# Kernel optimization log

Hardware: AMD Instinct MI355X
Metric: run time of the kernel (lower is better)

## Reference

```python
import jax, jax.numpy as jnp
import numpy as np

B, T, C, H, KV, D = 2, 2048, 1024, 16, 4, 64
VE_GATE_CH = 32


def _rope(x, cos, sin):
    # x: (B,T,h,D); cos/sin: (1,T,1,D//2); half-split rotary
    d = x.shape[-1] // 2
    x1, x2 = x[..., :d], x[..., d:]
    return jnp.concatenate([x1 * cos + x2 * sin, -x1 * sin + x2 * cos], axis=-1)


def _rms_norm(x, eps=1.1920929e-07):
    # F.rms_norm with no weight; eps defaults to finfo(fp32).eps
    return x * jax.lax.rsqrt(jnp.mean(x * x, axis=-1, keepdims=True) + eps)


def setup_inputs() -> dict:
    key = jax.random.key(0)
    ks = jax.random.split(key, 8)
    x = jax.random.normal(ks[0], (B, T, C), dtype=jnp.float32)
    ve = jax.random.normal(ks[1], (B, T, KV * D), dtype=jnp.float32)
    # standard RoPE tables, half-dim = D//2
    inv_freq = 1.0 / (10000.0 ** (np.arange(0, D, 2, dtype=np.float32) / D))  # (32,)
    freqs = np.arange(T, dtype=np.float32)[:, None] * inv_freq[None, :]       # (T,32)
    cos = jnp.asarray(np.cos(freqs))[None, :, None, :]
    sin = jnp.asarray(np.sin(freqs))[None, :, None, :]
    s = 0.02
    Wq = jax.random.normal(ks[2], (C, H * D), dtype=jnp.float32) * s
    Wk = jax.random.normal(ks[3], (C, KV * D), dtype=jnp.float32) * s
    Wv = jax.random.normal(ks[4], (C, KV * D), dtype=jnp.float32) * s
    Wo = jax.random.normal(ks[5], (C, C), dtype=jnp.float32) * s
    Wg = jax.random.normal(ks[6], (VE_GATE_CH, KV), dtype=jnp.float32) * s
    return {"x": x, "ve": ve, "cos": cos, "sin": sin,
            "Wq": Wq, "Wk": Wk, "Wv": Wv, "Wo": Wo, "Wg": Wg,
            "window": 1024}


def reference(x, ve, cos, sin, Wq, Wk, Wv, Wo, Wg, window):
    b, t, c = x.shape
    q = (x @ Wq).reshape(b, t, H, D)
    k = (x @ Wk).reshape(b, t, KV, D)
    v = (x @ Wv).reshape(b, t, KV, D)
    # value-embedding gating: gate = 2*sigmoid(x[..., :32] @ Wg)
    gate = 2.0 * jax.nn.sigmoid(x[..., :VE_GATE_CH] @ Wg)  # (B,T,KV)
    v = v + gate[..., None] * ve.reshape(b, t, KV, D)
    q = _rms_norm(_rope(q, cos, sin))
    k = _rms_norm(_rope(k, cos, sin))
    # GQA: repeat_interleave kv heads to match query heads
    groups = H // KV
    k = jnp.repeat(k, groups, axis=2)  # (B,T,H,D)
    v = jnp.repeat(v, groups, axis=2)
    scale = 1.0 / jnp.sqrt(jnp.asarray(D, dtype=q.dtype))
    scores = jnp.einsum("bthd,bshd->bhts", q, k) * scale  # (B,H,T,T)
    rows = jnp.arange(t)[:, None]
    cols = jnp.arange(t)[None, :]
    mask = (cols <= rows) & (cols > rows - window)  # causal sliding window
    scores = jnp.where(mask[None, None], scores, jnp.finfo(scores.dtype).min)
    attn = jax.nn.softmax(scores, axis=-1)
    y = jnp.einsum("bhts,bshd->bthd", attn, v).reshape(b, t, c)
    return y @ Wo
```

## Files before the change

kernel.cpp:

```cpp
#include <hip/hip_runtime.h>
#include <hip/hip_bf16.h>

#define B_ 2
#define T_ 2048
#define C_ 1024
#define H_ 16
#define KV_ 4
#define D_ 64
#define M_ (B_*T_)

typedef __attribute__((ext_vector_type(4))) float f32x4;
typedef __attribute__((ext_vector_type(8))) short bf16x8;

__device__ __forceinline__ float exp2fast(float x) {
  return __builtin_amdgcn_exp2f(x);
}

__device__ __forceinline__ unsigned short f2bfu(float f) {
  unsigned u = __builtin_bit_cast(unsigned, f);
  u += 0x7FFFu + ((u >> 16) & 1u);
  return (unsigned short)(u >> 16);
}

__device__ __forceinline__ short f2bf(float f) {
  return (short)f2bfu(f);
}

__device__ __forceinline__ float bf2f(short s) {
  unsigned u = ((unsigned)(unsigned short)s) << 16;
  return __builtin_bit_cast(float, u);
}

__device__ __forceinline__ unsigned cvtpk(float a, float b) {
  unsigned r;
  asm("v_cvt_pk_bf16_f32 %0, %1, %2" : "=v"(r) : "v"(a), "v"(b));
  return r;
}

__device__ __forceinline__ void gld_lds16(const void* g, void* l) {
  __builtin_amdgcn_global_load_lds(
      (const __attribute__((address_space(1))) void*)g,
      (__attribute__((address_space(3))) void*)l, 16, 0, 0);
}

__global__ __launch_bounds__(256) void k_cast(const float* __restrict__ in,
                                              short* __restrict__ out, int n) {
  int i = (blockIdx.x * 256 + threadIdx.x) * 4;
  if (i + 3 < n) {
    float4 f = *(const float4*)(in + i);
    short4 s;
    s.x = f2bf(f.x); s.y = f2bf(f.y); s.z = f2bf(f.z); s.w = f2bf(f.w);
    *(short4*)(out + i) = s;
  }
}

__global__ __launch_bounds__(256) void k_transpose_all(const float* __restrict__ Wq,
                                                       const float* __restrict__ Wk,
                                                       const float* __restrict__ Wv,
                                                       const float* __restrict__ Wo,
                                                       short* __restrict__ wT,
                                                       short* __restrict__ woT) {
  __shared__ float tile[32][33];
  int bx = blockIdx.x;
  const float* in; short* out; int Ncol, cb;
  if (bx < 32)      { in = Wq; out = wT;                       Ncol = 1024; cb = bx; }
  else if (bx < 40) { in = Wk; out = wT + (size_t)1024 * 1024; Ncol = 256;  cb = bx - 32; }
  else if (bx < 48) { in = Wv; out = wT + (size_t)1280 * 1024; Ncol = 256;  cb = bx - 40; }
  else              { in = Wo; out = woT;                      Ncol = 1024; cb = bx - 48; }
  const int R = 1024;
  int c0 = cb * 32, r0 = blockIdx.y * 32;
  int tx = threadIdx.x, ty = threadIdx.y;
#pragma unroll
  for (int i = 0; i < 32; i += 8)
    tile[ty + i][tx] = in[(size_t)(r0 + ty + i) * Ncol + c0 + tx];
  __syncthreads();
#pragma unroll
  for (int i = 0; i < 32; i += 8)
    out[(size_t)(c0 + ty + i) * R + r0 + tx] = f2bf(tile[tx][ty + i]);
}

__global__ __launch_bounds__(256) void k_gemm64(const short* __restrict__ A,
                                                const short* __restrict__ Bt,
                                                float* __restrict__ C,
                                                int M, int N, int K) {
  __shared__ short sA[64 * 64];
  __shared__ short sB[128 * 64];
  const int tid = threadIdx.x;
  const int wid = tid >> 6, lane = tid & 63;
  const int g = lane >> 4, c = lane & 15;
  const int wm = wid >> 1, wn = wid & 1;
  const int m0 = blockIdx.y * 64, n0 = blockIdx.x * 128;
  const int strow = tid >> 3;
  const int scol  = ((tid & 7) ^ (strow & 7)) * 8;
  const int sw = c & 7;

  const short* Ag = A + (size_t)(m0 + strow) * K + scol;
  const short* Bg = Bt + (size_t)(n0 + strow) * K + scol;
  const int ldbase = wid * 512;

  f32x4 acc[2][4] = {};

  for (int k0 = 0; k0 < K; k0 += 64) {
#pragma unroll
    for (int i = 0; i < 2; ++i)
      gld_lds16(Ag + (size_t)(i * 32) * K + k0, &sA[i * 2048 + ldbase]);
#pragma unroll
    for (int i = 0; i < 4; ++i)
      gld_lds16(Bg + (size_t)(i * 32) * K + k0, &sB[i * 2048 + ldbase]);
    __syncthreads();
#pragma unroll
    for (int kk = 0; kk < 2; ++kk) {
      bf16x8 af[2], bfr[4];
#pragma unroll
      for (int i = 0; i < 2; ++i)
        af[i] = *(const bf16x8*)&sA[(wm * 32 + i * 16 + c) * 64 + ((kk * 4 + g) ^ sw) * 8];
#pragma unroll
      for (int j = 0; j < 4; ++j)
        bfr[j] = *(const bf16x8*)&sB[(wn * 64 + j * 16 + c) * 64 + ((kk * 4 + g) ^ sw) * 8];
#pragma unroll
      for (int i = 0; i < 2; ++i)
#pragma unroll
        for (int j = 0; j < 4; ++j)
          acc[i][j] = __builtin_amdgcn_mfma_f32_16x16x32_bf16(af[i], bfr[j], acc[i][j], 0, 0, 0);
    }
    __syncthreads();
  }
#pragma unroll
  for (int i = 0; i < 2; ++i)
#pragma unroll
    for (int j = 0; j < 4; ++j) {
      int row = m0 + wm * 32 + i * 16 + g * 4;
      int col = n0 + wn * 64 + j * 16 + c;
      float* cp = C + (size_t)row * N + col;
#pragma unroll
      for (int r = 0; r < 4; ++r) cp[(size_t)r * N] = acc[i][j][r];
    }
}

__global__ __launch_bounds__(256) void k_gemm64b(const short* __restrict__ A,
                                                 const short* __restrict__ Bt,
                                                 short* __restrict__ C,
                                                 int M, int N, int K) {
  __shared__ short sA[64 * 64];
  __shared__ short sB[128 * 64];
  const int tid = threadIdx.x;
  const int wid = tid >> 6, lane = tid & 63;
  const int g = lane >> 4, c = lane & 15;
  const int wm = wid >> 1, wn = wid & 1;
  const int m0 = blockIdx.y * 64, n0 = blockIdx.x * 128;
  const int strow = tid >> 3;
  const int scol  = ((tid & 7) ^ (strow & 7)) * 8;
  const int sw = c & 7;

  const short* Ag = A + (size_t)(m0 + strow) * K + scol;
  const short* Bg = Bt + (size_t)(n0 + strow) * K + scol;
  const int ldbase = wid * 512;

  f32x4 acc[2][4] = {};

  for (int k0 = 0; k0 < K; k0 += 64) {
#pragma unroll
    for (int i = 0; i < 2; ++i)
      gld_lds16(Ag + (size_t)(i * 32) * K + k0, &sA[i * 2048 + ldbase]);
#pragma unroll
    for (int i = 0; i < 4; ++i)
      gld_lds16(Bg + (size_t)(i * 32) * K + k0, &sB[i * 2048 + ldbase]);
    __syncthreads();
#pragma unroll
    for (int kk = 0; kk < 2; ++kk) {
      bf16x8 af[2], bfr[4];
#pragma unroll
      for (int i = 0; i < 2; ++i)
        af[i] = *(const bf16x8*)&sA[(wm * 32 + i * 16 + c) * 64 + ((kk * 4 + g) ^ sw) * 8];
#pragma unroll
      for (int j = 0; j < 4; ++j)
        bfr[j] = *(const bf16x8*)&sB[(wn * 64 + j * 16 + c) * 64 + ((kk * 4 + g) ^ sw) * 8];
#pragma unroll
      for (int i = 0; i < 2; ++i)
#pragma unroll
        for (int j = 0; j < 4; ++j)
          acc[i][j] = __builtin_amdgcn_mfma_f32_16x16x32_bf16(af[i], bfr[j], acc[i][j], 0, 0, 0);
    }
    __syncthreads();
  }
#pragma unroll
  for (int i = 0; i < 2; ++i)
#pragma unroll
    for (int j = 0; j < 4; ++j) {
      int row = m0 + wm * 32 + i * 16 + g * 4;
      int col = n0 + wn * 64 + j * 16 + c;
      short* cp = C + (size_t)row * N + col;
#pragma unroll
      for (int r = 0; r < 4; ++r) cp[(size_t)r * N] = f2bf(acc[i][j][r]);
    }
}

__global__ __launch_bounds__(256) void k_post(const short* __restrict__ qkvb,
                                              const float* __restrict__ x,
                                              const float* __restrict__ cosp,
                                              const float* __restrict__ sinp,
                                              const float* __restrict__ Wg,
                                              short* __restrict__ qb,
                                              short* __restrict__ kb,
                                              float* __restrict__ gateb) {
  const int row = blockIdx.x;
  const int b = row >> 11, t = row & (T_ - 1);
  const int wid = threadIdx.x >> 6, lane = threadIdx.x & 63;
  const short* qrow = qkvb + (size_t)row * 1536;
  const float cv = cosp[t * 32 + (lane & 31)];
  const float sv = sinp[t * 32 + (lane & 31)];

  for (int vi = wid; vi < 24; vi += 4) {
    if (vi < 20) {
      float val = bf2f(qrow[vi < 16 ? vi * 64 + lane : 1024 + (vi - 16) * 64 + lane]);
      float other = __shfl_xor(val, 32);
      float r = (lane < 32) ? fmaf(val, cv, other * sv) : fmaf(val, cv, -other * sv);
      float ss = r * r;
      ss += __shfl_xor(ss, 1);  ss += __shfl_xor(ss, 2);  ss += __shfl_xor(ss, 4);
      ss += __shfl_xor(ss, 8);  ss += __shfl_xor(ss, 16); ss += __shfl_xor(ss, 32);
      float outv = r * rsqrtf(ss * (1.0f / 64.0f) + 1.1920929e-07f);
      if (vi < 16)
        qb[((size_t)(b * H_ + vi) * T_ + t) * D_ + lane] = f2bf(outv);
      else
        kb[((size_t)(b * KV_ + (vi - 16)) * T_ + t) * D_ + lane] = f2bf(outv);
    } else {
      int kvh = vi - 20;
      float xg = (lane < 32) ? x[(size_t)row * C_ + lane] * Wg[lane * KV_ + kvh] : 0.0f;
      xg += __shfl_xor(xg, 1);  xg += __shfl_xor(xg, 2);  xg += __shfl_xor(xg, 4);
      xg += __shfl_xor(xg, 8);  xg += __shfl_xor(xg, 16); xg += __shfl_xor(xg, 32);
      if (lane == 0)
        gateb[(size_t)row * KV_ + kvh] = 2.0f / (1.0f + __expf(-xg));
    }
  }
}

__global__ __launch_bounds__(256) void k_vtrans(const short* __restrict__ qkvb,
                                                const float* __restrict__ ve,
                                                const float* __restrict__ gateb,
                                                short* __restrict__ vT) {
  const int t0 = blockIdx.x * 64;
  const int bk = blockIdx.y;
  const int b = bk >> 2, kv = bk & 3;
  const int tx = threadIdx.x;
  const int ty = threadIdx.y;
  __shared__ float tile[64][65];
#pragma unroll
  for (int i = 0; i < 16; ++i) {
    const int tr = ty + 4 * i;
    const int row = b * T_ + t0 + tr;
    float g = gateb[(size_t)row * KV_ + kv];
    float v = bf2f(qkvb[(size_t)row * 1536 + 1280 + kv * 64 + tx]);
    v = fmaf(g, ve[(size_t)row * (KV_ * D_) + kv * 64 + tx], v);
    tile[tr][tx] = v;
  }
  __syncthreads();
#pragma unroll
  for (int i = 0; i < 16; ++i) {
    const int d = ty + 4 * i;
    vT[((size_t)bk * 64 + d) * T_ + t0 + tx] = f2bf(tile[tx][d]);
  }
}

__global__ __launch_bounds__(512, 6) void k_attn(const short* __restrict__ qg,
                                                 const short* __restrict__ kg,
                                                 const short* __restrict__ vg,
                                                 short* __restrict__ yb,
                                                 const int* __restrict__ winp) {
  const int wsz = *winp;
  const int qt = blockIdx.x, bh = blockIdx.y;
  const int b = bh >> 4, h = bh & 15;
  const int kvh = h >> 2;
  const int tid = threadIdx.x;
  const int wid = tid >> 6, lane = tid & 63;
  const int g = lane >> 4, c = lane & 15;
  const int t0 = qt * 128 + wid * 16;

  __shared__ short sK[2][64 * 64];
  __shared__ short sV[2][64 * 64];
  __shared__ short spt_all[8][16][72];
  short (*spt)[72] = spt_all[wid];

  const short* qbase = qg + ((size_t)(b * H_ + h) * T_ + t0) * D_;
  const bf16x8 bq0 = *(const bf16x8*)(qbase + c * D_ + g * 8);
  const bf16x8 bq1 = *(const bf16x8*)(qbase + c * D_ + 32 + g * 8);
  const short* kbase = kg + (size_t)(b * KV_ + kvh) * T_ * D_;
  const short* vbase = vg + (size_t)(b * KV_ + kvh) * D_ * T_;

  const int srow0 = tid >> 3;
  const int sq    = ((tid & 7) ^ (srow0 & 7)) * 8;
  const int ldst0 = wid * 512;

  float m = -20000.0f, l = 0.0f;
  f32x4 o[4] = {};

  int lo = t0 - wsz + 1; if (lo < 0) lo = 0;
  const int kt_lo_w = lo >> 6;
  const int kt_hi_w = (t0 + 15) >> 6;
  int lou = qt * 128 - wsz + 1; if (lou < 0) lou = 0;
  const int kt_lo_u = lou >> 6;
  const int kt_hi_u = 2 * qt + 1;
  const int qgl = t0 + c;
  const float SC2 = 0.125f * 1.44269504088896340736f;

  {
    const short* ksrc = kbase + (size_t)(kt_lo_u * 64 + srow0) * D_ + sq;
    gld_lds16(ksrc, &sK[0][ldst0]);
    const short* vsrc = vbase + (size_t)srow0 * T_ + kt_lo_u * 64 + sq;
    gld_lds16(vsrc, &sV[0][ldst0]);
  }
  __syncthreads();

  int cb = 0;
  for (int kt = kt_lo_u; kt <= kt_hi_u; ++kt) {
    const int kc0 = kt * 64;
    if (kt < kt_hi_u) {
      const short* ksrc = kbase + (size_t)((kt + 1) * 64 + srow0) * D_ + sq;
      gld_lds16(ksrc, &sK[cb ^ 1][ldst0]);
      const short* vsrc = vbase + (size_t)srow0 * T_ + (kt + 1) * 64 + sq;
      gld_lds16(vsrc, &sV[cb ^ 1][ldst0]);
    }
    if (kt >= kt_lo_w && kt <= kt_hi_w) {
      f32x4 s[4] = {};
#pragma unroll
      for (int cj = 0; cj < 4; ++cj) {
        const int rbase = (cj * 16 + c) * 64;
        const int sw = (c & 7);
        bf16x8 k0 = *(const bf16x8*)&sK[cb][rbase + ((g ^ sw) * 8)];
        bf16x8 k1 = *(const bf16x8*)&sK[cb][rbase + (((4 + g) ^ sw) * 8)];
        s[cj] = __builtin_amdgcn_mfma_f32_16x16x32_bf16(k0, bq0, s[cj], 0, 0, 0);
        s[cj] = __builtin_amdgcn_mfma_f32_16x16x32_bf16(k1, bq1, s[cj], 0, 0, 0);
      }
      const bool edge = (kt >= kt_hi_w) || (kt <= kt_lo_w + 1);
      float tmax = -3.0e38f;
#pragma unroll
      for (int cj = 0; cj < 4; ++cj)
#pragma unroll
        for (int r = 0; r < 4; ++r) {
          float v = s[cj][r];
          if (edge) {
            int kv = kc0 + cj * 16 + 4 * g + r;
            v = (kv <= qgl && kv > qgl - wsz) ? v : -1.0e9f;
            s[cj][r] = v;
          }
          tmax = fmaxf(tmax, v);
        }
      tmax = fmaxf(tmax, __shfl_xor(tmax, 16));
      tmax = fmaxf(tmax, __shfl_xor(tmax, 32));
      const float tms = tmax * SC2;
      if (!__all(tms <= m + 8.0f)) {
        const float nm = fmaxf(m, tms);
        const float fr = exp2fast(m - nm);
        m = nm;
        l *= fr;
#pragma unroll
        for (int nd = 0; nd < 4; ++nd)
#pragma unroll
          for (int r = 0; r < 4; ++r) o[nd][r] *= fr;
      }
      const float negm = -m;
      float psum = 0.0f;
      unsigned pb[8];
#pragma unroll
      for (int cj = 0; cj < 4; ++cj) {
        float p0 = exp2fast(fmaf(s[cj][0], SC2, negm));
        float p1 = exp2fast(fmaf(s[cj][1], SC2, negm));
        float p2 = exp2fast(fmaf(s[cj][2], SC2, negm));
        float p3 = exp2fast(fmaf(s[cj][3], SC2, negm));
        psum += (p0 + p1) + (p2 + p3);
        pb[2 * cj]     = cvtpk(p0, p1);
        pb[2 * cj + 1] = cvtpk(p2, p3);
      }
      psum += __shfl_xor(psum, 16);
      psum += __shfl_xor(psum, 32);
      l += psum;
#pragma unroll
      for (int cj = 0; cj < 4; ++cj) {
        unsigned long long w = ((unsigned long long)pb[2 * cj + 1] << 32) | pb[2 * cj];
        *(unsigned long long*)&spt[c][cj * 16 + 4 * g] = w;
      }
      asm volatile("s_waitcnt lgkmcnt(0)" ::: "memory");
#pragma unroll
      for (int ks = 0; ks < 2; ++ks) {
        bf16x8 bp = *(const bf16x8*)&spt[c][ks * 32 + g * 8];
#pragma unroll
        for (int nd = 0; nd < 4; ++nd) {
          const int rbase = (nd * 16 + c) * 64;
          bf16x8 bv = *(const bf16x8*)&sV[cb][rbase + (((ks * 4 + g) ^ (c & 7)) * 8)];
          o[nd] = __builtin_amdgcn_mfma_f32_16x16x32_bf16(bv, bp, o[nd], 0, 0, 0);
        }
      }
    }
    __syncthreads();
    cb ^= 1;
  }
  const float inv = 1.0f / l;
#pragma unroll
  for (int nd = 0; nd < 4; ++nd) {
    unsigned d0 = cvtpk(o[nd][0] * inv, o[nd][1] * inv);
    unsigned d1 = cvtpk(o[nd][2] * inv, o[nd][3] * inv);
    unsigned long long w = ((unsigned long long)d1 << 32) | d0;
    *(unsigned long long*)(yb + ((size_t)b * T_ + t0 + c) * C_ + h * D_ + nd * 16 + 4 * g) = w;
  }
}

extern "C" void kernel_launch(void* const* d_in, const int* in_sizes, int n_in,
                              void* d_out, int out_size, void* d_ws, size_t ws_size,
                              hipStream_t stream) {
  const float* x    = (const float*)d_in[0];
  const float* ve   = (const float*)d_in[1];
  const float* cosp = (const float*)d_in[2];
  const float* sinp = (const float*)d_in[3];
  const float* Wq   = (const float*)d_in[4];
  const float* Wk   = (const float*)d_in[5];
  const float* Wv   = (const float*)d_in[6];
  const float* Wo   = (const float*)d_in[7];
  const float* Wg   = (const float*)d_in[8];
  const int*   winp = (const int*)d_in[9];
  float* out = (float*)d_out;
  char* ws = (char*)d_ws;

  const size_t MB = 1024 * 1024;
  short* xb    = (short*)(ws);
  short* wT    = (short*)(ws + 8  * MB);
  short* woT   = (short*)(ws + 11 * MB);
  short* qkvb  = (short*)(ws + 13 * MB);
  short* qb    = (short*)(ws + 25 * MB);
  short* kbuf  = (short*)(ws + 33 * MB);
  short* vT    = (short*)(ws + 35 * MB);
  short* yb    = (short*)(ws + 37 * MB);
  float* gateb = (float*)(ws + 45 * MB);

  k_cast<<<4096, 256, 0, stream>>>(x, xb, M_ * C_);
  k_transpose_all<<<dim3(80, 32), dim3(32, 8), 0, stream>>>(Wq, Wk, Wv, Wo, wT, woT);

  k_gemm64b<<<dim3(12, 64), 256, 0, stream>>>(xb, wT, qkvb, M_, 1536, 1024);
  k_post<<<4096, 256, 0, stream>>>(qkvb, x, cosp, sinp, Wg, qb, kbuf, gateb);
  k_vtrans<<<dim3(32, 8), dim3(64, 4), 0, stream>>>(qkvb, ve, gateb, vT);
  k_attn<<<dim3(16, 32), 512, 0, stream>>>(qb, kbuf, vT, yb, winp);
  k_gemm64<<<dim3(8, 64), 256, 0, stream>>>(yb, woT, out, M_, 1024, 1024);
}
```

Measured before the change: 110.2 us.

## Give each attention wave two query sub-tiles to reuse K/V fragments

The attention kernel now runs 4 waves of 256 threads instead of 8 waves of 512, and each wave handles 32 query rows as two 16-row sub-tiles. Each K and V fragment read from LDS feeds two MFMAs, which halves LDS reads per query. Each thread now issues two global-to-LDS loads per tile to keep K/V staging complete. It also adds s_setprio around the MFMA sections and reverses the query-tile order for half of the head blocks to balance work. The costs are more registers (two sets of softmax state and accumulators) and fewer waves per block to hide latency.

```diff
diff --git a/kernel.cpp b/kernel.cpp
--- a/kernel.cpp
+++ b/kernel.cpp
@@ -261,28 +261,34 @@
   }
 }
 
-__global__ __launch_bounds__(512, 6) void k_attn(const short* __restrict__ qg,
+__global__ __launch_bounds__(256, 4) void k_attn(const short* __restrict__ qg,
                                                  const short* __restrict__ kg,
                                                  const short* __restrict__ vg,
                                                  short* __restrict__ yb,
                                                  const int* __restrict__ winp) {
   const int wsz = *winp;
-  const int qt = blockIdx.x, bh = blockIdx.y;
+  const int y = blockIdx.y;
+  const int qt = (y < 16) ? blockIdx.x : 15 - blockIdx.x;
+  const int bh = y;
   const int b = bh >> 4, h = bh & 15;
   const int kvh = h >> 2;
   const int tid = threadIdx.x;
   const int wid = tid >> 6, lane = tid & 63;
   const int g = lane >> 4, c = lane & 15;
-  const int t0 = qt * 128 + wid * 16;
+  const int t0 = qt * 128 + wid * 32;
 
   __shared__ short sK[2][64 * 64];
   __shared__ short sV[2][64 * 64];
-  __shared__ short spt_all[8][16][72];
+  __shared__ short spt_all[4][32][72];
   short (*spt)[72] = spt_all[wid];
 
   const short* qbase = qg + ((size_t)(b * H_ + h) * T_ + t0) * D_;
-  const bf16x8 bq0 = *(const bf16x8*)(qbase + c * D_ + g * 8);
-  const bf16x8 bq1 = *(const bf16x8*)(qbase + c * D_ + 32 + g * 8);
+  bf16x8 bq[2][2];
+#pragma unroll
+  for (int qbi = 0; qbi < 2; ++qbi)
+#pragma unroll
+    for (int kh = 0; kh < 2; ++kh)
+      bq[qbi][kh] = *(const bf16x8*)(qbase + (size_t)(qbi * 16 + c) * D_ + kh * 32 + g * 8);
   const short* kbase = kg + (size_t)(b * KV_ + kvh) * T_ * D_;
   const short* vbase = vg + (size_t)(b * KV_ + kvh) * D_ * T_;
 
@@ -290,23 +296,25 @@
   const int sq    = ((tid & 7) ^ (srow0 & 7)) * 8;
   const int ldst0 = wid * 512;
 
-  float m = -20000.0f, l = 0.0f;
-  f32x4 o[4] = {};
+  float m0 = -20000.0f, m1 = -20000.0f, l0 = 0.0f, l1 = 0.0f;
+  f32x4 o[2][4] = {};
 
   int lo = t0 - wsz + 1; if (lo < 0) lo = 0;
   const int kt_lo_w = lo >> 6;
-  const int kt_hi_w = (t0 + 15) >> 6;
+  const int kt_hi_w = (t0 + 31) >> 6;
   int lou = qt * 128 - wsz + 1; if (lou < 0) lou = 0;
   const int kt_lo_u = lou >> 6;
   const int kt_hi_u = 2 * qt + 1;
-  const int qgl = t0 + c;
+  const int qgl0 = t0 + c, qgl1 = t0 + 16 + c;
   const float SC2 = 0.125f * 1.44269504088896340736f;
 
   {
     const short* ksrc = kbase + (size_t)(kt_lo_u * 64 + srow0) * D_ + sq;
-    gld_lds16(ksrc, &sK[0][ldst0]);
+    gld_lds16(ksrc,                   &sK[0][ldst0]);
+    gld_lds16(ksrc + (size_t)32 * D_, &sK[0][ldst0 + 2048]);
     const short* vsrc = vbase + (size_t)srow0 * T_ + kt_lo_u * 64 + sq;
-    gld_lds16(vsrc, &sV[0][ldst0]);
+    gld_lds16(vsrc,                   &sV[0][ldst0]);
+    gld_lds16(vsrc + (size_t)32 * T_, &sV[0][ldst0 + 2048]);
   }
   __syncthreads();
 
@@ -315,91 +323,120 @@
     const int kc0 = kt * 64;
     if (kt < kt_hi_u) {
       const short* ksrc = kbase + (size_t)((kt + 1) * 64 + srow0) * D_ + sq;
-      gld_lds16(ksrc, &sK[cb ^ 1][ldst0]);
+      gld_lds16(ksrc,                   &sK[cb ^ 1][ldst0]);
+      gld_lds16(ksrc + (size_t)32 * D_, &sK[cb ^ 1][ldst0 + 2048]);
       const short* vsrc = vbase + (size_t)srow0 * T_ + (kt + 1) * 64 + sq;
-      gld_lds16(vsrc, &sV[cb ^ 1][ldst0]);
+      gld_lds16(vsrc,                   &sV[cb ^ 1][ldst0]);
+      gld_lds16(vsrc + (size_t)32 * T_, &sV[cb ^ 1][ldst0 + 2048]);
     }
     if (kt >= kt_lo_w && kt <= kt_hi_w) {
-      f32x4 s[4] = {};
+      f32x4 s[2][4] = {};
+      __builtin_amdgcn_s_setprio(1);
 #pragma unroll
       for (int cj = 0; cj < 4; ++cj) {
         const int rbase = (cj * 16 + c) * 64;
         const int sw = (c & 7);
         bf16x8 k0 = *(const bf16x8*)&sK[cb][rbase + ((g ^ sw) * 8)];
         bf16x8 k1 = *(const bf16x8*)&sK[cb][rbase + (((4 + g) ^ sw) * 8)];
-        s[cj] = __builtin_amdgcn_mfma_f32_16x16x32_bf16(k0, bq0, s[cj], 0, 0, 0);
-        s[cj] = __builtin_amdgcn_mfma_f32_16x16x32_bf16(k1, bq1, s[cj], 0, 0, 0);
+        s[0][cj] = __builtin_amdgcn_mfma_f32_16x16x32_bf16(k0, bq[0][0], s[0][cj], 0, 0, 0);
+        s[0][cj] = __builtin_amdgcn_mfma_f32_16x16x32_bf16(k1, bq[0][1], s[0][cj], 0, 0, 0);
+        s[1][cj] = __builtin_amdgcn_mfma_f32_16x16x32_bf16(k0, bq[1][0], s[1][cj], 0, 0, 0);
+        s[1][cj] = __builtin_amdgcn_mfma_f32_16x16x32_bf16(k1, bq[1][1], s[1][cj], 0, 0, 0);
       }
+      __builtin_amdgcn_s_setprio(0);
       const bool edge = (kt >= kt_hi_w) || (kt <= kt_lo_w + 1);
-      float tmax = -3.0e38f;
+      float tmax0 = -3.0e38f, tmax1 = -3.0e38f;
 #pragma unroll
       for (int cj = 0; cj < 4; ++cj)
 #pragma unroll
         for (int r = 0; r < 4; ++r) {
-          float v = s[cj][r];
+          float v0 = s[0][cj][r], v1 = s[1][cj][r];
           if (edge) {
             int kv = kc0 + cj * 16 + 4 * g + r;
-            v = (kv <= qgl && kv > qgl - wsz) ? v : -1.0e9f;
-            s[cj][r] = v;
+            v0 = (kv <= qgl0 && kv > qgl0 - wsz) ? v0 : -1.0e9f;
+            v1 = (kv <= qgl1 && kv > qgl1 - wsz) ? v1 : -1.0e9f;
+            s[0][cj][r] = v0;
+            s[1][cj][r] = v1;
           }
-          tmax = fmaxf(tmax, v);
+          tmax0 = fmaxf(tmax0, v0);
+          tmax1 = fmaxf(tmax1, v1);
         }
-      tmax = fmaxf(tmax, __shfl_xor(tmax, 16));
-      tmax = fmaxf(tmax, __shfl_xor(tmax, 32));
-      const float tms = tmax * SC2;
-      if (!__all(tms <= m + 8.0f)) {
-        const float nm = fmaxf(m, tms);
-        const float fr = exp2fast(m - nm);
-        m = nm;
-        l *= fr;
+      tmax0 = fmaxf(tmax0, __shfl_xor(tmax0, 16));
+      tmax0 = fmaxf(tmax0, __shfl_xor(tmax0, 32));
+      tmax1 = fmaxf(tmax1, __shfl_xor(tmax1, 16));
+      tmax1 = fmaxf(tmax1, __shfl_xor(tmax1, 32));
+      const float tms0 = tmax0 * SC2, tms1 = tmax1 * SC2;
+      if (!__all(tms0 <= m0 + 8.0f && tms1 <= m1 + 8.0f)) {
+        const float nm0 = fmaxf(m0, tms0), nm1 = fmaxf(m1, tms1);
+        const float fr0 = exp2fast(m0 - nm0), fr1 = exp2fast(m1 - nm1);
+        m0 = nm0; m1 = nm1;
+        l0 *= fr0; l1 *= fr1;
 #pragma unroll
         for (int nd = 0; nd < 4; ++nd)
 #pragma unroll
-          for (int r = 0; r < 4; ++r) o[nd][r] *= fr;
+          for (int r = 0; r < 4; ++r) { o[0][nd][r] *= fr0; o[1][nd][r] *= fr1; }
       }
-      const float negm = -m;
-      float psum = 0.0f;
-      unsigned pb[8];
+      const float ngm0 = -m0, ngm1 = -m1;
+      float ps0 = 0.0f, ps1 = 0.0f;
+      unsigned pb[2][8];
 #pragma unroll
       for (int cj = 0; cj < 4; ++cj) {
-        float p0 = exp2fast(fmaf(s[cj][0], SC2, negm));
-        float p1 = exp2fast(fmaf(s[cj][1], SC2, negm));
-        float p2 = exp2fast(fmaf(s[cj][2], SC2, negm));
-        float p3 = exp2fast(fmaf(s[cj][3], SC2, negm));
-        psum += (p0 + p1) + (p2 + p3);
-        pb[2 * cj]     = cvtpk(p0, p1);
-        pb[2 * cj + 1] = cvtpk(p2, p3);
+        float a0 = exp2fast(fmaf(s[0][cj][0], SC2, ngm0));
+        float a1 = exp2fast(fmaf(s[0][cj][1], SC2, ngm0));
+        float a2 = exp2fast(fmaf(s[0][cj][2], SC2, ngm0));
+        float a3 = exp2fast(fmaf(s[0][cj][3], SC2, ngm0));
+        ps0 += (a0 + a1) + (a2 + a3);
+        pb[0][2 * cj]     = cvtpk(a0, a1);
+        pb[0][2 * cj + 1] = cvtpk(a2, a3);
+        float b0 = exp2fast(fmaf(s[1][cj][0], SC2, ngm1));
+        float b1 = exp2fast(fmaf(s[1][cj][1], SC2, ngm1));
+        float b2 = exp2fast(fmaf(s[1][cj][2], SC2, ngm1));
+        float b3 = exp2fast(fmaf(s[1][cj][3], SC2, ngm1));
+        ps1 += (b0 + b1) + (b2 + b3);
+        pb[1][2 * cj]     = cvtpk(b0, b1);
+        pb[1][2 * cj + 1] = cvtpk(b2, b3);
       }
-      psum += __shfl_xor(psum, 16);
-      psum += __shfl_xor(psum, 32);
-      l += psum;
-#pragma unroll
-      for (int cj = 0; cj < 4; ++cj) {
-        unsigned long long w = ((unsigned long long)pb[2 * cj + 1] << 32) | pb[2 * cj];
-        *(unsigned long long*)&spt[c][cj * 16 + 4 * g] = w;
-      }
+      ps0 += __shfl_xor(ps0, 16);  ps0 += __shfl_xor(ps0, 32);
+      ps1 += __shfl_xor(ps1, 16);  ps1 += __shfl_xor(ps1, 32);
+      l0 += ps0;  l1 += ps1;
+#pragma unroll
+      for (int qbi = 0; qbi < 2; ++qbi)
+#pragma unroll
+        for (int cj = 0; cj < 4; ++cj) {
+          unsigned long long w =
+              ((unsigned long long)pb[qbi][2 * cj + 1] << 32) | pb[qbi][2 * cj];
+          *(unsigned long long*)&spt[qbi * 16 + c][cj * 16 + 4 * g] = w;
+        }
       asm volatile("s_waitcnt lgkmcnt(0)" ::: "memory");
+      __builtin_amdgcn_s_setprio(1);
 #pragma unroll
       for (int ks = 0; ks < 2; ++ks) {
-        bf16x8 bp = *(const bf16x8*)&spt[c][ks * 32 + g * 8];
+        bf16x8 bp0 = *(const bf16x8*)&spt[c][ks * 32 + g * 8];
+        bf16x8 bp1 = *(const bf16x8*)&spt[16 + c][ks * 32 + g * 8];
 #pragma unroll
         for (int nd = 0; nd < 4; ++nd) {
           const int rbase = (nd * 16 + c) * 64;
           bf16x8 bv = *(const bf16x8*)&sV[cb][rbase + (((ks * 4 + g) ^ (c & 7)) * 8)];
-          o[nd] = __builtin_amdgcn_mfma_f32_16x16x32_bf16(bv, bp, o[nd], 0, 0, 0);
+          o[0][nd] = __builtin_amdgcn_mfma_f32_16x16x32_bf16(bv, bp0, o[0][nd], 0, 0, 0);
+          o[1][nd] = __builtin_amdgcn_mfma_f32_16x16x32_bf16(bv, bp1, o[1][nd], 0, 0, 0);
         }
       }
+      __builtin_amdgcn_s_setprio(0);
     }
     __syncthreads();
     cb ^= 1;
   }
-  const float inv = 1.0f / l;
+  const float inv0 = 1.0f / l0, inv1 = 1.0f / l1;
 #pragma unroll
   for (int nd = 0; nd < 4; ++nd) {
-    unsigned d0 = cvtpk(o[nd][0] * inv, o[nd][1] * inv);
-    unsigned d1 = cvtpk(o[nd][2] * inv, o[nd][3] * inv);
+    unsigned d0 = cvtpk(o[0][nd][0] * inv0, o[0][nd][1] * inv0);
+    unsigned d1 = cvtpk(o[0][nd][2] * inv0, o[0][nd][3] * inv0);
     unsigned long long w = ((unsigned long long)d1 << 32) | d0;
     *(unsigned long long*)(yb + ((size_t)b * T_ + t0 + c) * C_ + h * D_ + nd * 16 + 4 * g) = w;
+    unsigned e0 = cvtpk(o[1][nd][0] * inv1, o[1][nd][1] * inv1);
+    unsigned e1 = cvtpk(o[1][nd][2] * inv1, o[1][nd][3] * inv1);
+    unsigned long long w2 = ((unsigned long long)e1 << 32) | e0;
+    *(unsigned long long*)(yb + ((size_t)b * T_ + t0 + 16 + c) * C_ + h * D_ + nd * 16 + 4 * g) = w2;
   }
 }
 
@@ -436,6 +473,6 @@
   k_gemm64b<<<dim3(12, 64), 256, 0, stream>>>(xb, wT, qkvb, M_, 1536, 1024);
   k_post<<<4096, 256, 0, stream>>>(qkvb, x, cosp, sinp, Wg, qb, kbuf, gateb);
   k_vtrans<<<dim3(32, 8), dim3(64, 4), 0, stream>>>(qkvb, ve, gateb, vT);
-  k_attn<<<dim3(16, 32), 512, 0, stream>>>(qb, kbuf, vT, yb, winp);
+  k_attn<<<dim3(16, 32), 256, 0, stream>>>(qb, kbuf, vT, yb, winp);
   k_gemm64<<<dim3(8, 64), 256, 0, stream>>>(yb, woT, out, M_, 1024, 1024);
 }
```

Result: slower. 117.0 us (+6.2%).

## Fuse RoPE and RMS norm into QKV GEMM epilogue, fold gate into vtrans

Applied to the files above, without the earlier changes.

Applies rotary embedding and RMS normalisation to the q and k heads directly in the QKV GEMM epilogue and writes them in head-major bf16 layout. This removes the separate post-processing kernel and its read-back of q/k from global memory. The sigmoid value-embedding gate is now computed inside the V transpose kernel, which drops the gate buffer. The epilogue relies on a permuted head-dimension layout shared by q and k, which keeps dot products unchanged but makes the stored layout non-obvious.

```diff
diff --git a/kernel.cpp b/kernel.cpp
--- a/kernel.cpp
+++ b/kernel.cpp
@@ -137,12 +137,16 @@
     }
 }
 
-__global__ __launch_bounds__(256) void k_gemm64b(const short* __restrict__ A,
-                                                 const short* __restrict__ Bt,
-                                                 short* __restrict__ C,
-                                                 int M, int N, int K) {
+__global__ __launch_bounds__(256) void k_gemm_qkv(const short* __restrict__ A,
+                                                  const short* __restrict__ Bt,
+                                                  short* __restrict__ qkvb,
+                                                  short* __restrict__ qb,
+                                                  short* __restrict__ kbb,
+                                                  const float* __restrict__ cosp,
+                                                  const float* __restrict__ sinp) {
   __shared__ short sA[64 * 64];
   __shared__ short sB[128 * 64];
+  const int N = 1536, K = 1024;
   const int tid = threadIdx.x;
   const int wid = tid >> 6, lane = tid & 63;
   const int g = lane >> 4, c = lane & 15;
@@ -183,60 +187,56 @@
     }
     __syncthreads();
   }
-#pragma unroll
-  for (int i = 0; i < 2; ++i)
-#pragma unroll
-    for (int j = 0; j < 4; ++j) {
-      int row = m0 + wm * 32 + i * 16 + g * 4;
-      int col = n0 + wn * 64 + j * 16 + c;
-      short* cp = C + (size_t)row * N + col;
-#pragma unroll
-      for (int r = 0; r < 4; ++r) cp[(size_t)r * N] = f2bf(acc[i][j][r]);
-    }
-}
-
-__global__ __launch_bounds__(256) void k_post(const short* __restrict__ qkvb,
-                                              const float* __restrict__ x,
-                                              const float* __restrict__ cosp,
-                                              const float* __restrict__ sinp,
-                                              const float* __restrict__ Wg,
-                                              short* __restrict__ qb,
-                                              short* __restrict__ kb,
-                                              float* __restrict__ gateb) {
-  const int row = blockIdx.x;
-  const int b = row >> 11, t = row & (T_ - 1);
-  const int wid = threadIdx.x >> 6, lane = threadIdx.x & 63;
-  const short* qrow = qkvb + (size_t)row * 1536;
-  const float cv = cosp[t * 32 + (lane & 31)];
-  const float sv = sinp[t * 32 + (lane & 31)];
-
-  for (int vi = wid; vi < 24; vi += 4) {
-    if (vi < 20) {
-      float val = bf2f(qrow[vi < 16 ? vi * 64 + lane : 1024 + (vi - 16) * 64 + lane]);
-      float other = __shfl_xor(val, 32);
-      float r = (lane < 32) ? fmaf(val, cv, other * sv) : fmaf(val, cv, -other * sv);
-      float ss = r * r;
-      ss += __shfl_xor(ss, 1);  ss += __shfl_xor(ss, 2);  ss += __shfl_xor(ss, 4);
-      ss += __shfl_xor(ss, 8);  ss += __shfl_xor(ss, 16); ss += __shfl_xor(ss, 32);
-      float outv = r * rsqrtf(ss * (1.0f / 64.0f) + 1.1920929e-07f);
-      if (vi < 16)
-        qb[((size_t)(b * H_ + vi) * T_ + t) * D_ + lane] = f2bf(outv);
-      else
-        kb[((size_t)(b * KV_ + (vi - 16)) * T_ + t) * D_ + lane] = f2bf(outv);
-    } else {
-      int kvh = vi - 20;
-      float xg = (lane < 32) ? x[(size_t)row * C_ + lane] * Wg[lane * KV_ + kvh] : 0.0f;
-      xg += __shfl_xor(xg, 1);  xg += __shfl_xor(xg, 2);  xg += __shfl_xor(xg, 4);
-      xg += __shfl_xor(xg, 8);  xg += __shfl_xor(xg, 16); xg += __shfl_xor(xg, 32);
-      if (lane == 0)
-        gateb[(size_t)row * KV_ + kvh] = 2.0f / (1.0f + __expf(-xg));
-    }
+
+  const int head = blockIdx.x * 2 + wn;
+  const int b = m0 >> 11;
+  const int tbase = (m0 & (T_ - 1)) + wm * 32;
+  if (head < 20) {
+    short* outbase = (head < 16)
+        ? qb  + ((size_t)(b * H_ + head) * T_) * D_
+        : kbb + ((size_t)(b * KV_ + (head - 16)) * T_) * D_;
+#pragma unroll
+    for (int i = 0; i < 2; ++i)
+#pragma unroll
+      for (int r = 0; r < 4; ++r) {
+        const int t = tbase + i * 16 + g * 4 + r;
+        const float ca = cosp[t * 32 + c],      sa = sinp[t * 32 + c];
+        const float cbv = cosp[t * 32 + 16 + c], sbv = sinp[t * 32 + 16 + c];
+        const float f0 = acc[i][0][r], f1 = acc[i][1][r];
+        const float f2 = acc[i][2][r], f3 = acc[i][3][r];
+        const float r0 = f0 * ca + f2 * sa;
+        const float r1 = f1 * cbv + f3 * sbv;
+        const float r2 = f2 * ca - f0 * sa;
+        const float r3 = f3 * cbv - f1 * sbv;
+        float ss = (r0 * r0 + r1 * r1) + (r2 * r2 + r3 * r3);
+        ss += __shfl_xor(ss, 1);
+        ss += __shfl_xor(ss, 2);
+        ss += __shfl_xor(ss, 4);
+        ss += __shfl_xor(ss, 8);
+        const float sc = rsqrtf(ss * (1.0f / 64.0f) + 1.1920929e-07f);
+        unsigned w0 = cvtpk(r0 * sc, r1 * sc);
+        unsigned w1 = cvtpk(r2 * sc, r3 * sc);
+        unsigned long long w = ((unsigned long long)w1 << 32) | w0;
+        *(unsigned long long*)(outbase + (size_t)t * D_ + c * 4) = w;
+      }
+  } else {
+#pragma unroll
+    for (int i = 0; i < 2; ++i)
+#pragma unroll
+      for (int j = 0; j < 4; ++j) {
+        int row = m0 + wm * 32 + i * 16 + g * 4;
+        int col = n0 + wn * 64 + j * 16 + c;
+        short* cp = qkvb + (size_t)row * N + col;
+#pragma unroll
+        for (int r = 0; r < 4; ++r) cp[(size_t)r * N] = f2bf(acc[i][j][r]);
+      }
   }
 }
 
 __global__ __launch_bounds__(256) void k_vtrans(const short* __restrict__ qkvb,
                                                 const float* __restrict__ ve,
-                                                const float* __restrict__ gateb,
+                                                const float* __restrict__ x,
+                                                const float* __restrict__ Wg,
                                                 short* __restrict__ vT) {
   const int t0 = blockIdx.x * 64;
   const int bk = blockIdx.y;
@@ -244,13 +244,23 @@
   const int tx = threadIdx.x;
   const int ty = threadIdx.y;
   __shared__ float tile[64][65];
+  __shared__ float sgate[64];
+  if (ty == 0) {
+    const int row = b * T_ + t0 + tx;
+    const float* xr = x + (size_t)row * C_;
+    float a = 0.0f;
+#pragma unroll 8
+    for (int kk = 0; kk < 32; ++kk) a = fmaf(xr[kk], Wg[kk * KV_ + kv], a);
+    sgate[tx] = 2.0f / (1.0f + __expf(-a));
+  }
+  __syncthreads();
 #pragma unroll
   for (int i = 0; i < 16; ++i) {
     const int tr = ty + 4 * i;
     const int row = b * T_ + t0 + tr;
-    float g = gateb[(size_t)row * KV_ + kv];
+    float gt = sgate[tr];
     float v = bf2f(qkvb[(size_t)row * 1536 + 1280 + kv * 64 + tx]);
-    v = fmaf(g, ve[(size_t)row * (KV_ * D_) + kv * 64 + tx], v);
+    v = fmaf(gt, ve[(size_t)row * (KV_ * D_) + kv * 64 + tx], v);
     tile[tr][tx] = v;
   }
   __syncthreads();
@@ -428,14 +438,12 @@
   short* kbuf  = (short*)(ws + 33 * MB);
   short* vT    = (short*)(ws + 35 * MB);
   short* yb    = (short*)(ws + 37 * MB);
-  float* gateb = (float*)(ws + 45 * MB);
 
   k_cast<<<4096, 256, 0, stream>>>(x, xb, M_ * C_);
   k_transpose_all<<<dim3(80, 32), dim3(32, 8), 0, stream>>>(Wq, Wk, Wv, Wo, wT, woT);
 
-  k_gemm64b<<<dim3(12, 64), 256, 0, stream>>>(xb, wT, qkvb, M_, 1536, 1024);
-  k_post<<<4096, 256, 0, stream>>>(qkvb, x, cosp, sinp, Wg, qb, kbuf, gateb);
-  k_vtrans<<<dim3(32, 8), dim3(64, 4), 0, stream>>>(qkvb, ve, gateb, vT);
+  k_gemm_qkv<<<dim3(12, 64), 256, 0, stream>>>(xb, wT, qkvb, qb, kbuf, cosp, sinp);
+  k_vtrans<<<dim3(32, 8), dim3(64, 4), 0, stream>>>(qkvb, ve, x, Wg, vT);
   k_attn<<<dim3(16, 32), 512, 0, stream>>>(qb, kbuf, vT, yb, winp);
   k_gemm64<<<dim3(8, 64), 256, 0, stream>>>(yb, woT, out, M_, 1024, 1024);
 }
```

Result: faster. 95.54 us (-13.3%).
